# Kernel tuning notes

Hardware: AMD Instinct MI355X
Metric: run time of the kernel (lower is better)

## Reference

```python
import jax, jax.numpy as jnp
import numpy as np

ALPHA = 0.2          # LeakyReLU negative slope
NEG_INF = -9e15      # mask value used by the torch module


def setup_inputs() -> dict:
    key = jax.random.key(0)
    k_x, k_adj, k_w, k_a = jax.random.split(key, 4)
    B, N, D, L = 8, 2048, 128, 3
    x = jax.random.normal(k_x, (B, N, D), dtype=jnp.float32)
    adj = jax.random.randint(k_adj, (B, N, N), 0, 2, dtype=jnp.int32)
    Wg = jax.random.normal(k_w, (L, D, D), dtype=jnp.float32) * 0.08  # ~Linear init scale
    bg = jnp.zeros((L, D), dtype=jnp.float32)
    attn_a = jax.random.normal(k_a, (L, 2 * D), dtype=jnp.float32) * 0.08
    return {"x": x, "adj": adj, "Wg": Wg, "bg": bg, "attn_a": attn_a}


def reference(x, adj, Wg, bg, attn_a):
    # x: [B,N,D], adj: [B,N,N] int, Wg: [L,D,D], bg: [L,D], attn_a: [L,2D]
    D = x.shape[-1]
    L = Wg.shape[0]
    mask = adj > 0
    for i in range(L):  # small fixed layer loop
        h = jax.nn.relu(x @ Wg[i] + bg[i])                       # [B,N,D]
        # a_input[b,i,j] = [h_i, h_j]; dot with a splits into two rank-1 terms,
        # avoiding the N*N*2D intermediate while computing identical math.
        s1 = h @ attn_a[i, :D]                                   # [B,N]
        s2 = h @ attn_a[i, D:]                                   # [B,N]
        e = jax.nn.leaky_relu(s1[:, :, None] + s2[:, None, :], ALPHA)  # [B,N,N]
        e = jnp.where(mask, e, NEG_INF)
        attn = jax.nn.softmax(e, axis=2)                         # masked softmax over neighbors
        # dropout p=0.0 -> identity
        x = x + jnp.einsum('bij,bjd->bid', attn, h)              # residual update
    return x
```

## Files before the change

### kernel.cpp

```cpp
#include <hip/hip_runtime.h>
#include <stdint.h>

typedef __attribute__((ext_vector_type(8))) short short8;
typedef __attribute__((ext_vector_type(4))) float f32x4;

__device__ __forceinline__ unsigned short f2bf(float f) {
    unsigned u = __float_as_uint(f);
    unsigned r = u + 0x7fffu + ((u >> 16) & 1u);
    return (unsigned short)(r >> 16);
}
__device__ __forceinline__ unsigned fenc(float f) {
    unsigned u = __float_as_uint(f);
    return (u & 0x80000000u) ? ~u : (u | 0x80000000u);
}
__device__ __forceinline__ float fdec(unsigned e) {
    unsigned u = (e & 0x80000000u) ? (e & 0x7fffffffu) : ~e;
    return __uint_as_float(u);
}

__global__ __launch_bounds__(256) void k_init(const float* __restrict__ xin,
                                              const float* __restrict__ Wf,
                                              float* __restrict__ xq,
                                              unsigned short* __restrict__ wTb,
                                              unsigned* __restrict__ s2mx) {
    int blk = blockIdx.x, tid = threadIdx.x;
    if (blk < 2048) {
        int e0 = (blk * 256 + tid) * 4;
        *(f32x4*)(xq + e0) = *(const f32x4*)(xin + e0);
    } else if (blk < 2240) {
        int c = (blk - 2048) * 256 + tid;
        int l = c >> 14, rem = c & 16383, n = rem >> 7, k = rem & 127;
        wTb[c] = f2bf(Wf[l * 16384 + k * 128 + n]);
    } else if (tid < 24) {
        s2mx[tid] = fenc(-3e38f);
    }
}

__global__ __launch_bounds__(256) void k_pack(const int* __restrict__ adj,
                                              unsigned long long* __restrict__ packed) {
    int w = (blockIdx.x * 256 + threadIdx.x) >> 6;
    int lane = threadIdx.x & 63;
    for (int k = 0; k < 64; k++) {
        int q = w * 64 + k;
        int row = q >> 5, wd = q & 31;
        int v = adj[row * 2048 + wd * 64 + lane];
        unsigned long long m = __ballot(v > 0);
        if (lane == 0) packed[q] = m;
    }
}

__global__ __launch_bounds__(256) void k_h(
    const float* __restrict__ xq, const unsigned short* __restrict__ wTb,
    const float* __restrict__ bF, const float* __restrict__ aF, int layer,
    unsigned short* __restrict__ hT, float* __restrict__ s1g,
    float* __restrict__ s2g, unsigned* __restrict__ s2mx)
{
    __shared__ short xs[64 * 136];
    __shared__ short wsb[128 * 136];
    __shared__ float s2blk[4];
    int blk = blockIdx.x, tid = threadIdx.x;
    int row0 = blk * 64, b = blk >> 5;
    int w = tid >> 6, lane = tid & 63, quad = lane >> 4, l15 = lane & 15;

    for (int c = tid; c < 1024; c += 256) {
        int r = c >> 4, kg = c & 15;
        const float* src = &xq[(row0 + r) * 128 + kg * 8];
        f32x4 v0 = *(const f32x4*)src;
        f32x4 v1 = *(const f32x4*)(src + 4);
        short8 o;
        o[0] = (short)f2bf(v0[0]); o[1] = (short)f2bf(v0[1]);
        o[2] = (short)f2bf(v0[2]); o[3] = (short)f2bf(v0[3]);
        o[4] = (short)f2bf(v1[0]); o[5] = (short)f2bf(v1[1]);
        o[6] = (short)f2bf(v1[2]); o[7] = (short)f2bf(v1[3]);
        *(short8*)&xs[r * 136 + kg * 8] = o;
    }
    const unsigned short* wl = wTb + layer * 16384;
    for (int c = tid; c < 2048; c += 256) {
        int n = c >> 4, kg = c & 15;
        *(short8*)&wsb[n * 136 + kg * 8] = *(const short8*)&wl[n * 128 + kg * 8];
    }
    __syncthreads();

    f32x4 acc[8];
#pragma unroll
    for (int t = 0; t < 8; t++) acc[t] = {0.f, 0.f, 0.f, 0.f};
#pragma unroll
    for (int ks = 0; ks < 4; ks++) {
        short8 af = *(const short8*)&xs[(w * 16 + l15) * 136 + ks * 32 + quad * 8];
#pragma unroll
        for (int t = 0; t < 8; t++) {
            short8 bf = *(const short8*)&wsb[(t * 16 + l15) * 136 + ks * 32 + quad * 8];
            acc[t] = __builtin_amdgcn_mfma_f32_16x16x32_bf16(af, bf, acc[t], 0, 0, 0);
        }
    }

    float s1p[4] = {0.f, 0.f, 0.f, 0.f}, s2p[4] = {0.f, 0.f, 0.f, 0.f};
#pragma unroll
    for (int t = 0; t < 8; t++) {
        int colg = t * 16 + l15;
        float bgf = bF[layer * 128 + colg];
        float a1 = aF[layer * 256 + colg];
        float a2 = aF[layer * 256 + 128 + colg];
#pragma unroll
        for (int r = 0; r < 4; r++) {
            float v = acc[t][r] + bgf;
            v = v > 0.f ? v : 0.f;
            acc[t][r] = v;
            s1p[r] = fmaf(v, a1, s1p[r]);
            s2p[r] = fmaf(v, a2, s2p[r]);
        }
    }
#pragma unroll
    for (int r = 0; r < 4; r++) {
#pragma unroll
        for (int off = 1; off < 16; off <<= 1) {
            s1p[r] += __shfl_xor(s1p[r], off, 64);
            s2p[r] += __shfl_xor(s2p[r], off, 64);
        }
    }
    if (l15 == 0) {
#pragma unroll
        for (int r = 0; r < 4; r++) {
            int rowg = row0 + w * 16 + quad * 4 + r;
            s1g[rowg] = s1p[r];
            s2g[rowg] = s2p[r];
        }
    }
    float mx = fmaxf(fmaxf(s2p[0], s2p[1]), fmaxf(s2p[2], s2p[3]));
    mx = fmaxf(mx, __shfl_xor(mx, 16, 64));
    mx = fmaxf(mx, __shfl_xor(mx, 32, 64));
    if (lane == 0) s2blk[w] = mx;
    __syncthreads();

    short* st = (short*)wsb;
#pragma unroll
    for (int t = 0; t < 8; t++)
#pragma unroll
        for (int r = 0; r < 4; r++)
            st[(w * 16 + quad * 4 + r) * 130 + t * 16 + l15] = (short)f2bf(acc[t][r]);
    __syncthreads();
    if (tid == 0) {
        float m2 = fmaxf(fmaxf(s2blk[0], s2blk[1]), fmaxf(s2blk[2], s2blk[3]));
        atomicMax(&s2mx[layer * 8 + b], fenc(m2));
    }
    int i0 = (blk & 31) * 64;
    for (int c = tid; c < 1024; c += 256) {
        int d = c >> 3, ig = c & 7;
        short8 o;
#pragma unroll
        for (int ii = 0; ii < 8; ii++) o[ii] = st[(ig * 8 + ii) * 130 + d];
        *(short8*)&hT[(b * 128 + d) * 2048 + i0 + ig * 8] = o;
    }
}

__global__ __launch_bounds__(256) void k_attn(
    const unsigned long long* __restrict__ packed,
    const unsigned short* __restrict__ hT, const float* __restrict__ s1g,
    const float* __restrict__ s2g, const unsigned* __restrict__ s2mx,
    int layer, float* __restrict__ Opart, float* __restrict__ Ppart)
{
    __shared__ short ht[144 * 72];
    __shared__ unsigned long long bits[64 * 32];
    int blk = blockIdx.x, tid = threadIdx.x;
    int half = blk & 1, brow = blk >> 1;
    int b = brow >> 5;
    int rowg0 = brow * 64;
    int w = tid >> 6, lane = tid & 63, quad = lane >> 4, l15 = lane & 15;

    for (int c = tid; c < 2048; c += 256) bits[c] = packed[rowg0 * 32 + c];
    for (int c = tid; c < 128; c += 256) {
        int d = 128 + (c >> 3), jg = c & 7;
        short8 v;
        short one = (short)0x3F80;
        if (d == 128) { v[0]=one;v[1]=one;v[2]=one;v[3]=one;v[4]=one;v[5]=one;v[6]=one;v[7]=one; }
        else { v[0]=0;v[1]=0;v[2]=0;v[3]=0;v[4]=0;v[5]=0;v[6]=0;v[7]=0; }
        *(short8*)&ht[d * 72 + jg * 8] = v;
    }

    int rowA = w * 16 + l15;
    float s1v = s1g[rowg0 + rowA];
    float s2m = fdec(s2mx[layer * 8 + b]);
    float tmh = s1v + s2m;
    float mhat = fmaxf(tmh, 0.2f * tmh);
    f32x4 acc[9];
#pragma unroll
    for (int t = 0; t < 9; t++) acc[t] = {0.f, 0.f, 0.f, 0.f};

    int sd[4], sjg[4];
#pragma unroll
    for (int s = 0; s < 4; s++) {
        int c = tid + 256 * s;
        sd[s] = c >> 3; sjg[s] = c & 7;
    }
    short8 pv[4];
#pragma unroll
    for (int s = 0; s < 4; s++) {
        int jts = half * 16;
        pv[s] = *(const short8*)&hT[(b * 128 + sd[s]) * 2048 + jts * 64 + sjg[s] * 8];
    }

    const float* s2b = s2g + b * 2048;
    for (int it = 0; it < 16; it++) {
#pragma unroll
        for (int s = 0; s < 4; s++)
            *(short8*)&ht[sd[s] * 72 + sjg[s] * 8] = pv[s];
        __syncthreads();
        if (it < 15) {
#pragma unroll
            for (int s = 0; s < 4; s++) {
                int jts = half * 16 + it + 1;
                pv[s] = *(const short8*)&hT[(b * 128 + sd[s]) * 2048 + jts * 64 + sjg[s] * 8];
            }
        }
        int jt = half * 16 + it;
        unsigned long long word = bits[rowA * 32 + jt];
#pragma unroll
        for (int ks = 0; ks < 2; ks++) {
            unsigned b8 = (unsigned)(word >> (ks * 32 + quad * 8)) & 0xffu;
            int jbase = jt * 64 + ks * 32 + quad * 8;
            f32x4 sa = *(const f32x4*)&s2b[jbase];
            f32x4 sb = *(const f32x4*)&s2b[jbase + 4];
            float sv[8] = {sa[0], sa[1], sa[2], sa[3], sb[0], sb[1], sb[2], sb[3]};
            short8 af;
#pragma unroll
            for (int jj = 0; jj < 8; jj++) {
                float e = s1v + sv[jj];
                e = fmaxf(e, 0.2f * e);
                float pvv = __expf(e - mhat);
                pvv = (b8 & (1u << jj)) ? pvv : 0.f;
                af[jj] = (short)f2bf(pvv);
            }
#pragma unroll
            for (int t = 0; t < 9; t++) {
                short8 bf = *(const short8*)&ht[(t * 16 + l15) * 72 + ks * 32 + quad * 8];
                acc[t] = __builtin_amdgcn_mfma_f32_16x16x32_bf16(af, bf, acc[t], 0, 0, 0);
            }
        }
        __syncthreads();
    }

#pragma unroll
    for (int r = 0; r < 4; r++) {
        int rowgC = rowg0 + w * 16 + quad * 4 + r;
        float psum = __shfl(acc[8][r], lane & 48, 64);
        if (l15 == 0) Ppart[half * 16384 + rowgC] = psum;
#pragma unroll
        for (int t = 0; t < 8; t++)
            Opart[((size_t)half * 16384 + rowgC) * 128 + t * 16 + l15] = acc[t][r];
    }
}

__global__ __launch_bounds__(256) void k_comb(
    const float* __restrict__ Opart, const float* __restrict__ Ppart,
    float* __restrict__ xq)
{
    int idx = blockIdx.x * 256 + threadIdx.x;
    int row = idx >> 5;
    float p = Ppart[row] + Ppart[16384 + row];
    float rl = p > 0.f ? 1.0f / p : 0.f;
    f32x4 o0 = *(const f32x4*)&Opart[(size_t)idx * 4];
    f32x4 o1 = *(const f32x4*)&Opart[(size_t)idx * 4 + 2097152];
    f32x4 xv = *(const f32x4*)&xq[idx * 4];
#pragma unroll
    for (int k = 0; k < 4; k++) xv[k] += (o0[k] + o1[k]) * rl;
    *(f32x4*)&xq[idx * 4] = xv;
}

extern "C" void kernel_launch(void* const* d_in, const int* in_sizes, int n_in,
                              void* d_out, int out_size, void* d_ws, size_t ws_size,
                              hipStream_t stream) {
    const void* px = d_in[0];
    int ia = 1; long amax = -1;
    for (int i = 1; i < n_in; i++)
        if ((long)in_sizes[i] > amax) { amax = in_sizes[i]; ia = i; }
    int rem[8]; int m = 0;
    for (int i = 1; i < n_in && m < 8; i++) if (i != ia) rem[m++] = i;
    for (int i = 0; i < m; i++)
        for (int j = i + 1; j < m; j++)
            if (in_sizes[rem[j]] > in_sizes[rem[i]]) { int t = rem[i]; rem[i] = rem[j]; rem[j] = t; }
    const int*   padj = (const int*)((n_in > 1) ? d_in[ia] : d_in[0]);
    const float* pW = (const float*)((m > 0) ? d_in[rem[0]] : d_in[0]);
    const float* pa = (const float*)((m > 1) ? d_in[rem[1]] : d_in[0]);
    const float* pb = (const float*)((m > 2) ? d_in[rem[2]] : d_in[0]);

    float* xq = (float*)d_out;
    char* ws = (char*)d_ws;
    unsigned long long* packed = (unsigned long long*)ws;
    unsigned short* hT = (unsigned short*)(ws + 4194304);
    float* s1 = (float*)(ws + 8388608);
    float* s2 = (float*)(ws + 8454144);
    unsigned* s2mx = (unsigned*)(ws + 8519680);
    unsigned short* wTb = (unsigned short*)(ws + 8519808);
    float* Opart = (float*)(ws + 16777216);
    float* Ppart = (float*)(ws + 33554432);

    k_init<<<2241, 256, 0, stream>>>((const float*)px, pW, xq, wTb, s2mx);
    k_pack<<<2048, 256, 0, stream>>>(padj, packed);
    for (int l = 0; l < 3; l++) {
        k_h<<<256, 256, 0, stream>>>(xq, wTb, pb, pa, l, hT, s1, s2, s2mx);
        k_attn<<<512, 256, 0, stream>>>(packed, hT, s1, s2, s2mx, l, Opart, Ppart);
        k_comb<<<2048, 256, 0, stream>>>(Opart, Ppart, xq);
    }
}
```

Before: 368.5 us.

## Split attention K-range across waves and load hT fragments directly from global

Restructures k_attn so each block handles 32 rows and each of its 4 waves covers a quarter of the neighbor range, so the split-K partials grow from two to four. hT fragments are now read straight from global memory into registers instead of being staged through shared memory, which removes the per-iteration barriers and LDS traffic. The row-sum column becomes a constant ones operand. The cost is more partial outputs to write and combine in k_comb, and uncoalesced 16-byte global loads of hT that depend on cache reuse.

```diff
diff --git a/kernel.cpp b/kernel.cpp
--- a/kernel.cpp
+++ b/kernel.cpp
@@ -159,95 +159,88 @@
     const float* __restrict__ s2g, const unsigned* __restrict__ s2mx,
     int layer, float* __restrict__ Opart, float* __restrict__ Ppart)
 {
-    __shared__ short ht[144 * 72];
-    __shared__ unsigned long long bits[64 * 32];
+    __shared__ unsigned long long bits_t[32 * 32];
     int blk = blockIdx.x, tid = threadIdx.x;
-    int half = blk & 1, brow = blk >> 1;
-    int b = brow >> 5;
-    int rowg0 = brow * 64;
+    int b = blk >> 6;
+    int rowg0 = blk * 32;
     int w = tid >> 6, lane = tid & 63, quad = lane >> 4, l15 = lane & 15;
 
-    for (int c = tid; c < 2048; c += 256) bits[c] = packed[rowg0 * 32 + c];
-    for (int c = tid; c < 128; c += 256) {
-        int d = 128 + (c >> 3), jg = c & 7;
-        short8 v;
+    for (int c = tid; c < 1024; c += 256) {
+        int r = c >> 5, jt = c & 31;
+        bits_t[jt * 32 + r] = packed[(rowg0 + r) * 32 + jt];
+    }
+
+    float s2m = fdec(s2mx[layer * 8 + b]);
+    float s1v[2], mhat[2];
+#pragma unroll
+    for (int s = 0; s < 2; s++) {
+        s1v[s] = s1g[rowg0 + s * 16 + l15];
+        float tmh = s1v[s] + s2m;
+        mhat[s] = fmaxf(tmh, 0.2f * tmh);
+    }
+    f32x4 acc[2][9];
+#pragma unroll
+    for (int s = 0; s < 2; s++)
+#pragma unroll
+        for (int t = 0; t < 9; t++) acc[s][t] = {0.f, 0.f, 0.f, 0.f};
+
+    short8 onesf;
+    {
         short one = (short)0x3F80;
-        if (d == 128) { v[0]=one;v[1]=one;v[2]=one;v[3]=one;v[4]=one;v[5]=one;v[6]=one;v[7]=one; }
-        else { v[0]=0;v[1]=0;v[2]=0;v[3]=0;v[4]=0;v[5]=0;v[6]=0;v[7]=0; }
-        *(short8*)&ht[d * 72 + jg * 8] = v;
-    }
-
-    int rowA = w * 16 + l15;
-    float s1v = s1g[rowg0 + rowA];
-    float s2m = fdec(s2mx[layer * 8 + b]);
-    float tmh = s1v + s2m;
-    float mhat = fmaxf(tmh, 0.2f * tmh);
-    f32x4 acc[9];
-#pragma unroll
-    for (int t = 0; t < 9; t++) acc[t] = {0.f, 0.f, 0.f, 0.f};
-
-    int sd[4], sjg[4];
-#pragma unroll
-    for (int s = 0; s < 4; s++) {
-        int c = tid + 256 * s;
-        sd[s] = c >> 3; sjg[s] = c & 7;
-    }
-    short8 pv[4];
-#pragma unroll
-    for (int s = 0; s < 4; s++) {
-        int jts = half * 16;
-        pv[s] = *(const short8*)&hT[(b * 128 + sd[s]) * 2048 + jts * 64 + sjg[s] * 8];
-    }
+        short v = (l15 == 0) ? one : (short)0;
+        onesf[0]=v;onesf[1]=v;onesf[2]=v;onesf[3]=v;onesf[4]=v;onesf[5]=v;onesf[6]=v;onesf[7]=v;
+    }
+    __syncthreads();
 
     const float* s2b = s2g + b * 2048;
-    for (int it = 0; it < 16; it++) {
-#pragma unroll
-        for (int s = 0; s < 4; s++)
-            *(short8*)&ht[sd[s] * 72 + sjg[s] * 8] = pv[s];
-        __syncthreads();
-        if (it < 15) {
-#pragma unroll
-            for (int s = 0; s < 4; s++) {
-                int jts = half * 16 + it + 1;
-                pv[s] = *(const short8*)&hT[(b * 128 + sd[s]) * 2048 + jts * 64 + sjg[s] * 8];
-            }
-        }
-        int jt = half * 16 + it;
-        unsigned long long word = bits[rowA * 32 + jt];
+    const unsigned short* hTb = hT + (size_t)b * 128 * 2048;
+
+    for (int jl = 0; jl < 8; jl++) {
+        int jt = w * 8 + jl;
+        unsigned long long word0 = bits_t[jt * 32 + l15];
+        unsigned long long word1 = bits_t[jt * 32 + 16 + l15];
 #pragma unroll
         for (int ks = 0; ks < 2; ks++) {
-            unsigned b8 = (unsigned)(word >> (ks * 32 + quad * 8)) & 0xffu;
             int jbase = jt * 64 + ks * 32 + quad * 8;
+            short8 bfr[8];
+#pragma unroll
+            for (int t = 0; t < 8; t++)
+                bfr[t] = *(const short8*)&hTb[(t * 16 + l15) * 2048 + jbase];
             f32x4 sa = *(const f32x4*)&s2b[jbase];
             f32x4 sb = *(const f32x4*)&s2b[jbase + 4];
             float sv[8] = {sa[0], sa[1], sa[2], sa[3], sb[0], sb[1], sb[2], sb[3]};
-            short8 af;
-#pragma unroll
-            for (int jj = 0; jj < 8; jj++) {
-                float e = s1v + sv[jj];
-                e = fmaxf(e, 0.2f * e);
-                float pvv = __expf(e - mhat);
-                pvv = (b8 & (1u << jj)) ? pvv : 0.f;
-                af[jj] = (short)f2bf(pvv);
+#pragma unroll
+            for (int s = 0; s < 2; s++) {
+                unsigned long long word = s ? word1 : word0;
+                unsigned b8 = (unsigned)(word >> (ks * 32 + quad * 8)) & 0xffu;
+                short8 af;
+#pragma unroll
+                for (int jj = 0; jj < 8; jj++) {
+                    float e = s1v[s] + sv[jj];
+                    e = fmaxf(e, 0.2f * e);
+                    float pvv = __expf(e - mhat[s]);
+                    pvv = (b8 & (1u << jj)) ? pvv : 0.f;
+                    af[jj] = (short)f2bf(pvv);
+                }
+#pragma unroll
+                for (int t = 0; t < 8; t++)
+                    acc[s][t] = __builtin_amdgcn_mfma_f32_16x16x32_bf16(af, bfr[t], acc[s][t], 0, 0, 0);
+                acc[s][8] = __builtin_amdgcn_mfma_f32_16x16x32_bf16(af, onesf, acc[s][8], 0, 0, 0);
             }
-#pragma unroll
-            for (int t = 0; t < 9; t++) {
-                short8 bf = *(const short8*)&ht[(t * 16 + l15) * 72 + ks * 32 + quad * 8];
-                acc[t] = __builtin_amdgcn_mfma_f32_16x16x32_bf16(af, bf, acc[t], 0, 0, 0);
-            }
-        }
-        __syncthreads();
-    }
-
-#pragma unroll
-    for (int r = 0; r < 4; r++) {
-        int rowgC = rowg0 + w * 16 + quad * 4 + r;
-        float psum = __shfl(acc[8][r], lane & 48, 64);
-        if (l15 == 0) Ppart[half * 16384 + rowgC] = psum;
-#pragma unroll
-        for (int t = 0; t < 8; t++)
-            Opart[((size_t)half * 16384 + rowgC) * 128 + t * 16 + l15] = acc[t][r];
-    }
+        }
+    }
+
+#pragma unroll
+    for (int s = 0; s < 2; s++)
+#pragma unroll
+        for (int r = 0; r < 4; r++) {
+            int rowgC = rowg0 + s * 16 + quad * 4 + r;
+            float psum = __shfl(acc[s][8][r], lane & 48, 64);
+            if (l15 == 0) Ppart[w * 16384 + rowgC] = psum;
+#pragma unroll
+            for (int t = 0; t < 8; t++)
+                Opart[((size_t)w * 16384 + rowgC) * 128 + t * 16 + l15] = acc[s][t][r];
+        }
 }
 
 __global__ __launch_bounds__(256) void k_comb(
@@ -256,13 +249,15 @@
 {
     int idx = blockIdx.x * 256 + threadIdx.x;
     int row = idx >> 5;
-    float p = Ppart[row] + Ppart[16384 + row];
+    float p = Ppart[row] + Ppart[16384 + row] + Ppart[32768 + row] + Ppart[49152 + row];
     float rl = p > 0.f ? 1.0f / p : 0.f;
     f32x4 o0 = *(const f32x4*)&Opart[(size_t)idx * 4];
     f32x4 o1 = *(const f32x4*)&Opart[(size_t)idx * 4 + 2097152];
+    f32x4 o2 = *(const f32x4*)&Opart[(size_t)idx * 4 + 4194304];
+    f32x4 o3 = *(const f32x4*)&Opart[(size_t)idx * 4 + 6291456];
     f32x4 xv = *(const f32x4*)&xq[idx * 4];
 #pragma unroll
-    for (int k = 0; k < 4; k++) xv[k] += (o0[k] + o1[k]) * rl;
+    for (int k = 0; k < 4; k++) xv[k] += (o0[k] + o1[k] + o2[k] + o3[k]) * rl;
     *(f32x4*)&xq[idx * 4] = xv;
 }
 
@@ -292,7 +287,7 @@
     unsigned* s2mx = (unsigned*)(ws + 8519680);
     unsigned short* wTb = (unsigned short*)(ws + 8519808);
     float* Opart = (float*)(ws + 16777216);
-    float* Ppart = (float*)(ws + 33554432);
+    float* Ppart = (float*)(ws + 50331648);
 
     k_init<<<2241, 256, 0, stream>>>((const float*)px, pW, xq, wTb, s2mx);
     k_pack<<<2048, 256, 0, stream>>>(padj, packed);
```

Measured after the change: 394.7 us. 7.1% more time.
